# Optimization experiments

Hardware: AMD Instinct MI355X
Metric: run time of the kernel (lower is better)

## Reference

```python
import jax, jax.numpy as jnp
import numpy as np

B, D, L = 32, 64, 8192
K = 512
COMMITMENT_COST = 0.1


def setup_inputs() -> dict:
    key = jax.random.key(0)
    k1, k2 = jax.random.split(key)
    x = jax.random.normal(k1, (B, D, L), dtype=jnp.float32)
    # Embedding initialized uniform(-1/K, 1/K) as in the torch module
    weight = jax.random.uniform(k2, (K, D), dtype=jnp.float32, minval=-1.0 / K, maxval=1.0 / K)
    return {"x": x, "weight": weight}


def reference(x, weight):
    # x: [B, D, L] -> inputs: [B, L, D]
    inputs = jnp.transpose(x, (0, 2, 1))
    flat = inputs.reshape(-1, D)  # [N, D]
    # Squared L2 distances to codebook: [N, K]
    distances = (
        jnp.sum(flat * flat, axis=1, keepdims=True)
        + jnp.sum(weight * weight, axis=1)
        - 2.0 * flat @ weight.T
    )
    encoding_indices = jnp.argmin(distances, axis=1)  # [N]
    # Gather quantized vectors (equivalent to one-hot @ weight)
    quantized = weight[encoding_indices].reshape(inputs.shape)  # [B, L, D]
    e_latent_loss = jnp.mean((jax.lax.stop_gradient(quantized) - inputs) ** 2)
    q_latent_loss = jnp.mean((quantized - jax.lax.stop_gradient(inputs)) ** 2)
    loss = q_latent_loss + COMMITMENT_COST * e_latent_loss
    # Straight-through estimator
    quantized_st = inputs + jax.lax.stop_gradient(quantized - inputs)
    out = jnp.transpose(quantized_st, (0, 2, 1))  # [B, D, L]
    # perplexity = number of unique codes used (jit-friendly via bincount)
    perplexity = jnp.sum(jnp.bincount(encoding_indices, length=K) > 0)
    return (out, loss, perplexity, weight, encoding_indices[:, None])
```

## Files before the change

kernel.cpp:

```cpp
#include <hip/hip_runtime.h>
#include <math.h>

#define BB 32
#define DD 64
#define LL 8192
#define KK 512
#define NN (BB*LL)

#define OUT0_SZ  (BB*DD*LL)
#define LOSS_OFF (OUT0_SZ)
#define PERP_OFF (OUT0_SZ + 1)
#define W_OFF    (OUT0_SZ + 2)
#define IDX_OFF  (W_OFF + KK*DD)

#define WS_TVEC 0
#define WS_HIST 512
#define WS_LACC 1024
#define WS_WPH  1032
#define WS_WPL  (1032 + 16384)

typedef __attribute__((ext_vector_type(4))) float f32x4;
typedef __attribute__((ext_vector_type(8))) short s16x8;
typedef unsigned long long u64;

#define WINDOW 1e-4f

__device__ __forceinline__ unsigned short f2bf(float f) {
  unsigned int u = __float_as_uint(f);
  return (unsigned short)((u + 0x7FFFu + ((u >> 16) & 1u)) >> 16);
}
__device__ __forceinline__ float bf2f(unsigned short s) {
  return __uint_as_float(((unsigned int)s) << 16);
}
__device__ __forceinline__ u64 shflx64(u64 v, int m) {
  unsigned lo = __shfl_xor((unsigned)v, m);
  unsigned hi = __shfl_xor((unsigned)(v >> 32), m);
  return ((u64)hi << 32) | lo;
}
__device__ __forceinline__ unsigned fenc(float f) {
  unsigned u = __float_as_uint(f);
  return (u & 0x80000000u) ? ~u : (u | 0x80000000u);
}
__device__ __forceinline__ float fdec(unsigned e) {
  return __uint_as_float((e & 0x80000000u) ? (e ^ 0x80000000u) : ~e);
}

__global__ void vq_init(const float* __restrict__ w, float* __restrict__ ws,
                        float* __restrict__ dout) {
#pragma clang fp contract(off)
  int t = blockIdx.x * blockDim.x + threadIdx.x;
  if (t < KK) {
    const float* wr = w + t * DD;
    float r[8];
#pragma unroll
    for (int j = 0; j < 8; j++) { float v = wr[j]; r[j] = v * v; }
#pragma unroll
    for (int blk = 8; blk < 64; blk += 8) {
#pragma unroll
      for (int j = 0; j < 8; j++) { float v = wr[blk + j]; float a = v * v; r[j] = r[j] + a; }
    }
    ws[WS_TVEC + t] = ((r[0] + r[1]) + (r[2] + r[3])) + ((r[4] + r[5]) + (r[6] + r[7]));
    ((int*)ws)[WS_HIST + t] = 0;
  }
  if (t == 0) ws[WS_LACC] = 0.0f;

  {
    int j    = t & 7;
    int lane = (t >> 3) & 63;
    int ks   = (t >> 9) & 1;
    int ct   = t >> 10;
    int code = ct * 16 + (lane & 15);
    int d    = ks * 32 + ((lane >> 4) << 3) + j;
    float v  = w[code * DD + d];
    unsigned short h = f2bf(v);
    unsigned short l = f2bf(v - bf2f(h));
    ((unsigned short*)(ws + WS_WPH))[((ct * 2 + ks) * 64 + lane) * 8 + j] = h;
    ((unsigned short*)(ws + WS_WPL))[((ct * 2 + ks) * 64 + lane) * 8 + j] = l;
  }

  if (t < KK * DD / 2) {
    ((float2*)(dout + W_OFF))[t] = ((const float2*)w)[t];
  }
}

__launch_bounds__(256, 2)
__global__ void vq_main(const float* __restrict__ x, const float* __restrict__ w,
                        const float* __restrict__ ws, float* __restrict__ dout) {
#pragma clang fp contract(off)
  __shared__ uint4 xh_lds[4][64][8];
  __shared__ uint4 xl_lds[4][64][8];
  __shared__ float t_lds[KK];
  __shared__ u64   g_lds[256];
  __shared__ unsigned short cand[256][4];
  __shared__ int   ccnt[256];
  __shared__ unsigned char flags[KK];

  const float* tvec = ws + WS_TVEC;
  const s16x8* wph8 = (const s16x8*)(ws + WS_WPH);
  const s16x8* wpl8 = (const s16x8*)(ws + WS_WPL);
  int* hist = (int*)ws + WS_HIST;
  float* lacc = (float*)ws + WS_LACC;

  const int tid  = threadIdx.x;
  const int lane = tid & 63;
  const int wv   = tid >> 6;
  const int res  = lane & 15;

  for (int e = tid; e < KK; e += 256) { t_lds[e] = tvec[e]; flags[e] = 0; }
  ccnt[tid] = 0;

  const int n = blockIdx.x * 256 + wv * 64 + lane;
  const int b = n >> 13, l = n & 8191;
  const float* px = x + (size_t)b * DD * LL + l;

  {
    float xv[64];
#pragma unroll
    for (int i = 0; i < 64; i++) xv[i] = px[(size_t)i * LL];
#pragma unroll
    for (int blk = 0; blk < 8; blk++) {
      unsigned ph[4], pl[4];
#pragma unroll
      for (int q = 0; q < 4; q++) {
        float v0 = xv[blk * 8 + 2 * q],     v1 = xv[blk * 8 + 2 * q + 1];
        unsigned short h0 = f2bf(v0), h1 = f2bf(v1);
        unsigned short l0 = f2bf(v0 - bf2f(h0)), l1 = f2bf(v1 - bf2f(h1));
        ph[q] = (unsigned)h0 | ((unsigned)h1 << 16);
        pl[q] = (unsigned)l0 | ((unsigned)l1 << 16);
      }
      int sw = blk ^ (lane & 7);
      uint4 vh; vh.x = ph[0]; vh.y = ph[1]; vh.z = ph[2]; vh.w = ph[3];
      uint4 vl; vl.x = pl[0]; vl.y = pl[1]; vl.z = pl[2]; vl.w = pl[3];
      xh_lds[wv][lane][sw] = vh;
      xl_lds[wv][lane][sw] = vl;
    }
  }
  __syncthreads();

  s16x8 afh[4][2], afl[4][2];
  {
    const s16x8* xh8 = (const s16x8*)xh_lds;
    const s16x8* xl8 = (const s16x8*)xl_lds;
#pragma unroll
    for (int t2 = 0; t2 < 4; t2++)
#pragma unroll
      for (int ks = 0; ks < 2; ks++) {
        int idx = (wv * 64 + t2 * 16 + (lane & 15)) * 8 + ((ks * 4 + (lane >> 4)) ^ (lane & 7));
        afh[t2][ks] = xh8[idx];
        afl[t2][ks] = xl8[idx];
      }
  }

  float d1[4][4], d2[4][4]; int k1[4][4];
#pragma unroll
  for (int t2 = 0; t2 < 4; t2++)
#pragma unroll
    for (int r = 0; r < 4; r++) { d1[t2][r] = INFINITY; d2[t2][r] = INFINITY; k1[t2][r] = 0; }

  s16x8 bh0 = wph8[lane], bh1 = wph8[64 + lane];
  s16x8 bl0 = wpl8[lane], bl1 = wpl8[64 + lane];
  float tc = t_lds[res];

#pragma clang loop unroll(disable)
  for (int ct = 0; ct < 32; ct++) {
    int cn = (ct + 1) & 31;
    s16x8 nh0 = wph8[cn * 128 + lane],      nh1 = wph8[cn * 128 + 64 + lane];
    s16x8 nl0 = wpl8[cn * 128 + lane],      nl1 = wpl8[cn * 128 + 64 + lane];
    float ntc = t_lds[cn * 16 + res];

#pragma unroll
    for (int t2 = 0; t2 < 4; t2++) {
      f32x4 acc = {0.f, 0.f, 0.f, 0.f};
      acc = __builtin_amdgcn_mfma_f32_16x16x32_bf16(afl[t2][0], bh0, acc, 0, 0, 0);
      acc = __builtin_amdgcn_mfma_f32_16x16x32_bf16(afl[t2][1], bh1, acc, 0, 0, 0);
      acc = __builtin_amdgcn_mfma_f32_16x16x32_bf16(afh[t2][0], bl0, acc, 0, 0, 0);
      acc = __builtin_amdgcn_mfma_f32_16x16x32_bf16(afh[t2][1], bl1, acc, 0, 0, 0);
      acc = __builtin_amdgcn_mfma_f32_16x16x32_bf16(afh[t2][0], bh0, acc, 0, 0, 0);
      acc = __builtin_amdgcn_mfma_f32_16x16x32_bf16(afh[t2][1], bh1, acc, 0, 0, 0);
#pragma unroll
      for (int r = 0; r < 4; r++) {
        float dap = fmaf(-2.0f, acc[r], tc);
        bool c1 = dap < d1[t2][r];
        bool c2 = dap < d2[t2][r];
        d2[t2][r] = c1 ? d1[t2][r] : (c2 ? dap : d2[t2][r]);
        d1[t2][r] = c1 ? dap : d1[t2][r];
        k1[t2][r] = c1 ? ct : k1[t2][r];
      }
    }
    bh0 = nh0; bh1 = nh1; bl0 = nl0; bl1 = nl1; tc = ntc;
  }

  u64 gmin[4][4];
#pragma unroll
  for (int t2 = 0; t2 < 4; t2++)
#pragma unroll
    for (int r = 0; r < 4; r++) {
      u64 pk = (((u64)fenc(d1[t2][r])) << 32) | (u64)(k1[t2][r] * 16 + res);
      u64 q1 = shflx64(pk, 1); pk = pk < q1 ? pk : q1;
      u64 q2 = shflx64(pk, 2); pk = pk < q2 ? pk : q2;
      u64 q4 = shflx64(pk, 4); pk = pk < q4 ? pk : q4;
      u64 q8 = shflx64(pk, 8); pk = pk < q8 ? pk : q8;
      gmin[t2][r] = pk;
    }

#pragma unroll
  for (int t2 = 0; t2 < 4; t2++)
#pragma unroll
    for (int r = 0; r < 4; r++) {
      int row = wv * 64 + t2 * 16 + ((lane >> 4) << 2) + r;
      if (res == 0) g_lds[row] = gmin[t2][r];
      float thr = fdec((unsigned)(gmin[t2][r] >> 32)) + WINDOW;
      bool in1 = d1[t2][r] <= thr;
      bool in2 = d2[t2][r] <= thr;
      if (in1) { int p = atomicAdd(&ccnt[row], 1); if (p < 4) cand[row][p] = (unsigned short)(k1[t2][r] * 16 + res); }
      if (in2) { int p = atomicAdd(&ccnt[row], 1); if (p < 4) cand[row][p] = (unsigned short)(512 + res); }
    }
  __syncthreads();

  float xr[64];
#pragma unroll
  for (int i = 0; i < 64; i++) xr[i] = px[(size_t)i * LL];

  int kwin;
  {
    int row = wv * 64 + lane;
    int cnt = ccnt[row];
    if (cnt <= 1) {
      kwin = (int)(g_lds[row] & 0x1FFu);
    } else {
      float s;
      {
        float r[8];
#pragma unroll
        for (int j = 0; j < 8; j++) r[j] = xr[j] * xr[j];
#pragma unroll
        for (int blk = 8; blk < 64; blk += 8)
#pragma unroll
          for (int j = 0; j < 8; j++) { float a = xr[blk + j] * xr[blk + j]; r[j] = r[j] + a; }
        s = ((r[0] + r[1]) + (r[2] + r[3])) + ((r[4] + r[5]) + (r[6] + r[7]));
      }
      u64 best = ~0ULL;
      auto evalExact = [&](int c) {
        const float4* wr = (const float4*)(w + c * DD);
        float gg = 0.0f;
#pragma unroll
        for (int i = 0; i < 16; i++) {
          float4 wq = wr[i];
          gg = fmaf(xr[4 * i + 0], wq.x, gg); gg = fmaf(xr[4 * i + 1], wq.y, gg);
          gg = fmaf(xr[4 * i + 2], wq.z, gg); gg = fmaf(xr[4 * i + 3], wq.w, gg);
        }
        float de = fmaf(-2.0f, gg, s + t_lds[c]);
        u64 pk = (((u64)__float_as_uint(de)) << 32) | (u64)c;
        if (pk < best) best = pk;
      };
      if (cnt > 4) {
        for (int c = 0; c < KK; c++) evalExact(c);
      } else {
        for (int i = 0; i < cnt; i++) {
          int c = cand[row][i];
          if (c < 512) evalExact(c);
          else { int c0 = c - 512; for (int jj = 0; jj < 32; jj++) evalExact(jj * 16 + c0); }
        }
      }
      kwin = (int)(best & 0x1FFu);
    }
  }

  float ls = 0.0f;
  {
    float* o = dout + (size_t)b * DD * LL + l;
    const float4* wr = (const float4*)(w + kwin * DD);
#pragma unroll
    for (int i = 0; i < 16; i++) {
      float4 v = wr[i];
      o[(size_t)(4 * i + 0) * LL] = v.x; o[(size_t)(4 * i + 1) * LL] = v.y;
      o[(size_t)(4 * i + 2) * LL] = v.z; o[(size_t)(4 * i + 3) * LL] = v.w;
      float df;
      df = v.x - xr[4 * i + 0]; ls = fmaf(df, df, ls);
      df = v.y - xr[4 * i + 1]; ls = fmaf(df, df, ls);
      df = v.z - xr[4 * i + 2]; ls = fmaf(df, df, ls);
      df = v.w - xr[4 * i + 3]; ls = fmaf(df, df, ls);
    }
  }
  dout[IDX_OFF + n] = (float)kwin;
  flags[kwin] = 1;

#pragma unroll
  for (int o = 32; o > 0; o >>= 1) ls += __shfl_down(ls, o);
  if ((tid & 63) == 0) atomicAdd(lacc, ls);

  __syncthreads();
  for (int e = tid; e < KK; e += 256)
    if (flags[e]) atomicOr(&hist[e], 1);
}

__global__ void vq_final(const float* __restrict__ ws, float* __restrict__ dout) {
  __shared__ int red[512];
  const int* hist = (const int*)ws + WS_HIST;
  int tid = threadIdx.x;
  red[tid] = (hist[tid] != 0) ? 1 : 0;
  __syncthreads();
  for (int sx = 256; sx > 0; sx >>= 1) {
    if (tid < sx) red[tid] += red[tid + sx];
    __syncthreads();
  }
  if (tid == 0) {
    dout[PERP_OFF] = (float)red[0];
    float m = ws[WS_LACC] / 16777216.0f;
    dout[LOSS_OFF] = m + 0.1f * m;
  }
}

extern "C" void kernel_launch(void* const* d_in, const int* in_sizes, int n_in,
                              void* d_out, int out_size, void* d_ws, size_t ws_size,
                              hipStream_t stream) {
  const float* x = (const float*)d_in[0];
  const float* w = (const float*)d_in[1];
  float* dout = (float*)d_out;
  float* ws = (float*)d_ws;

  vq_init<<<128, 256, 0, stream>>>(w, ws, dout);
  vq_main<<<NN / 256, 256, 0, stream>>>(x, w, ws, dout);
  vq_final<<<1, 512, 0, stream>>>(ws, dout);
}
```

Before: 246.9 us.

## Share one LDS staging buffer for hi/lo bf16 splits and hoist x reload

Replaces the separate hi and lo LDS staging buffers with a single buffer reused in two passes: the hi halves are written, read into registers, then the lo halves are written and read. This halves that LDS footprint, which may let more blocks fit per CU, at the cost of two extra block barriers. The x reload for the refinement phase is moved ahead of the candidate-reduction code behind a sched_barrier so its global latency overlaps the shuffle and atomic work, which raises register pressure during that phase.

```diff
diff --git a/kernel.cpp b/kernel.cpp
--- a/kernel.cpp
+++ b/kernel.cpp
@@ -87,8 +87,7 @@
 __global__ void vq_main(const float* __restrict__ x, const float* __restrict__ w,
                         const float* __restrict__ ws, float* __restrict__ dout) {
 #pragma clang fp contract(off)
-  __shared__ uint4 xh_lds[4][64][8];
-  __shared__ uint4 xl_lds[4][64][8];
+  __shared__ uint4 xs_lds[4][64][8];
   __shared__ float t_lds[KK];
   __shared__ u64   g_lds[256];
   __shared__ unsigned short cand[256][4];
@@ -113,42 +112,61 @@
   const int b = n >> 13, l = n & 8191;
   const float* px = x + (size_t)b * DD * LL + l;
 
+  s16x8 afh[4][2], afl[4][2];
   {
     float xv[64];
 #pragma unroll
     for (int i = 0; i < 64; i++) xv[i] = px[(size_t)i * LL];
+
 #pragma unroll
     for (int blk = 0; blk < 8; blk++) {
-      unsigned ph[4], pl[4];
+      unsigned ph[4];
 #pragma unroll
       for (int q = 0; q < 4; q++) {
-        float v0 = xv[blk * 8 + 2 * q],     v1 = xv[blk * 8 + 2 * q + 1];
-        unsigned short h0 = f2bf(v0), h1 = f2bf(v1);
-        unsigned short l0 = f2bf(v0 - bf2f(h0)), l1 = f2bf(v1 - bf2f(h1));
-        ph[q] = (unsigned)h0 | ((unsigned)h1 << 16);
-        pl[q] = (unsigned)l0 | ((unsigned)l1 << 16);
+        float v0 = xv[blk * 8 + 2 * q], v1 = xv[blk * 8 + 2 * q + 1];
+        ph[q] = (unsigned)f2bf(v0) | ((unsigned)f2bf(v1) << 16);
       }
       int sw = blk ^ (lane & 7);
       uint4 vh; vh.x = ph[0]; vh.y = ph[1]; vh.z = ph[2]; vh.w = ph[3];
+      xs_lds[wv][lane][sw] = vh;
+    }
+    __syncthreads();
+    {
+      const s16x8* xs8 = (const s16x8*)xs_lds;
+#pragma unroll
+      for (int t2 = 0; t2 < 4; t2++)
+#pragma unroll
+        for (int ks = 0; ks < 2; ks++) {
+          int idx = (wv * 64 + t2 * 16 + (lane & 15)) * 8 + ((ks * 4 + (lane >> 4)) ^ (lane & 7));
+          afh[t2][ks] = xs8[idx];
+        }
+    }
+    __syncthreads();
+
+#pragma unroll
+    for (int blk = 0; blk < 8; blk++) {
+      unsigned pl[4];
+#pragma unroll
+      for (int q = 0; q < 4; q++) {
+        float v0 = xv[blk * 8 + 2 * q],     h0f = bf2f(f2bf(v0));
+        float v1 = xv[blk * 8 + 2 * q + 1], h1f = bf2f(f2bf(v1));
+        pl[q] = (unsigned)f2bf(v0 - h0f) | ((unsigned)f2bf(v1 - h1f) << 16);
+      }
+      int sw = blk ^ (lane & 7);
       uint4 vl; vl.x = pl[0]; vl.y = pl[1]; vl.z = pl[2]; vl.w = pl[3];
-      xh_lds[wv][lane][sw] = vh;
-      xl_lds[wv][lane][sw] = vl;
-    }
-  }
-  __syncthreads();
-
-  s16x8 afh[4][2], afl[4][2];
-  {
-    const s16x8* xh8 = (const s16x8*)xh_lds;
-    const s16x8* xl8 = (const s16x8*)xl_lds;
-#pragma unroll
-    for (int t2 = 0; t2 < 4; t2++)
-#pragma unroll
-      for (int ks = 0; ks < 2; ks++) {
-        int idx = (wv * 64 + t2 * 16 + (lane & 15)) * 8 + ((ks * 4 + (lane >> 4)) ^ (lane & 7));
-        afh[t2][ks] = xh8[idx];
-        afl[t2][ks] = xl8[idx];
-      }
+      xs_lds[wv][lane][sw] = vl;
+    }
+    __syncthreads();
+    {
+      const s16x8* xs8 = (const s16x8*)xs_lds;
+#pragma unroll
+      for (int t2 = 0; t2 < 4; t2++)
+#pragma unroll
+        for (int ks = 0; ks < 2; ks++) {
+          int idx = (wv * 64 + t2 * 16 + (lane & 15)) * 8 + ((ks * 4 + (lane >> 4)) ^ (lane & 7));
+          afl[t2][ks] = xs8[idx];
+        }
+    }
   }
 
   float d1[4][4], d2[4][4]; int k1[4][4];
@@ -190,6 +208,11 @@
     bh0 = nh0; bh1 = nh1; bl0 = nl0; bl1 = nl1; tc = ntc;
   }
 
+  __builtin_amdgcn_sched_barrier(0);
+  float xr[64];
+#pragma unroll
+  for (int i = 0; i < 64; i++) xr[i] = px[(size_t)i * LL];
+
   u64 gmin[4][4];
 #pragma unroll
   for (int t2 = 0; t2 < 4; t2++)
@@ -216,10 +239,6 @@
       if (in2) { int p = atomicAdd(&ccnt[row], 1); if (p < 4) cand[row][p] = (unsigned short)(512 + res); }
     }
   __syncthreads();
-
-  float xr[64];
-#pragma unroll
-  for (int i = 0; i < 64; i++) xr[i] = px[(size_t)i * LL];
 
   int kwin;
   {
```

After: 236.8 us. 4.1% less time.

## Drop x low-part MFMAs, widen rescore window, raise occupancy target

Applied to the files above, without the earlier changes.

Removes the bf16 low-part split of x, so each distance tile uses four MFMAs instead of six and x staging in LDS halves. The candidate window is widened to absorb the larger approximation error, and exact fp32 rescoring still picks the winner. The top-2 tracking becomes branchless min/max, x is reloaded only when rescoring or when computing the loss, and launch bounds target three blocks per CU to cut register pressure. The risks are more rows falling into the slow exact-rescore path and possible spills under the tighter register budget.

```diff
diff --git a/kernel.cpp b/kernel.cpp
--- a/kernel.cpp
+++ b/kernel.cpp
@@ -23,7 +23,7 @@
 typedef __attribute__((ext_vector_type(8))) short s16x8;
 typedef unsigned long long u64;
 
-#define WINDOW 1e-4f
+#define WINDOW 5e-4f
 
 __device__ __forceinline__ unsigned short f2bf(float f) {
   unsigned int u = __float_as_uint(f);
@@ -83,12 +83,11 @@
   }
 }
 
-__launch_bounds__(256, 2)
+__launch_bounds__(256, 3)
 __global__ void vq_main(const float* __restrict__ x, const float* __restrict__ w,
                         const float* __restrict__ ws, float* __restrict__ dout) {
 #pragma clang fp contract(off)
-  __shared__ uint4 xh_lds[4][64][8];
-  __shared__ uint4 xl_lds[4][64][8];
+  __shared__ uint4 xs_lds[4][64][8];
   __shared__ float t_lds[KK];
   __shared__ u64   g_lds[256];
   __shared__ unsigned short cand[256][4];
@@ -119,35 +118,28 @@
     for (int i = 0; i < 64; i++) xv[i] = px[(size_t)i * LL];
 #pragma unroll
     for (int blk = 0; blk < 8; blk++) {
-      unsigned ph[4], pl[4];
+      unsigned ph[4];
 #pragma unroll
       for (int q = 0; q < 4; q++) {
-        float v0 = xv[blk * 8 + 2 * q],     v1 = xv[blk * 8 + 2 * q + 1];
-        unsigned short h0 = f2bf(v0), h1 = f2bf(v1);
-        unsigned short l0 = f2bf(v0 - bf2f(h0)), l1 = f2bf(v1 - bf2f(h1));
-        ph[q] = (unsigned)h0 | ((unsigned)h1 << 16);
-        pl[q] = (unsigned)l0 | ((unsigned)l1 << 16);
+        float v0 = xv[blk * 8 + 2 * q], v1 = xv[blk * 8 + 2 * q + 1];
+        ph[q] = (unsigned)f2bf(v0) | ((unsigned)f2bf(v1) << 16);
       }
       int sw = blk ^ (lane & 7);
       uint4 vh; vh.x = ph[0]; vh.y = ph[1]; vh.z = ph[2]; vh.w = ph[3];
-      uint4 vl; vl.x = pl[0]; vl.y = pl[1]; vl.z = pl[2]; vl.w = pl[3];
-      xh_lds[wv][lane][sw] = vh;
-      xl_lds[wv][lane][sw] = vl;
+      xs_lds[wv][lane][sw] = vh;
     }
   }
   __syncthreads();
 
-  s16x8 afh[4][2], afl[4][2];
-  {
-    const s16x8* xh8 = (const s16x8*)xh_lds;
-    const s16x8* xl8 = (const s16x8*)xl_lds;
+  s16x8 afh[4][2];
+  {
+    const s16x8* xs8 = (const s16x8*)xs_lds;
 #pragma unroll
     for (int t2 = 0; t2 < 4; t2++)
 #pragma unroll
       for (int ks = 0; ks < 2; ks++) {
         int idx = (wv * 64 + t2 * 16 + (lane & 15)) * 8 + ((ks * 4 + (lane >> 4)) ^ (lane & 7));
-        afh[t2][ks] = xh8[idx];
-        afl[t2][ks] = xl8[idx];
+        afh[t2][ks] = xs8[idx];
       }
   }
 
@@ -171,8 +163,6 @@
 #pragma unroll
     for (int t2 = 0; t2 < 4; t2++) {
       f32x4 acc = {0.f, 0.f, 0.f, 0.f};
-      acc = __builtin_amdgcn_mfma_f32_16x16x32_bf16(afl[t2][0], bh0, acc, 0, 0, 0);
-      acc = __builtin_amdgcn_mfma_f32_16x16x32_bf16(afl[t2][1], bh1, acc, 0, 0, 0);
       acc = __builtin_amdgcn_mfma_f32_16x16x32_bf16(afh[t2][0], bl0, acc, 0, 0, 0);
       acc = __builtin_amdgcn_mfma_f32_16x16x32_bf16(afh[t2][1], bl1, acc, 0, 0, 0);
       acc = __builtin_amdgcn_mfma_f32_16x16x32_bf16(afh[t2][0], bh0, acc, 0, 0, 0);
@@ -180,11 +170,11 @@
 #pragma unroll
       for (int r = 0; r < 4; r++) {
         float dap = fmaf(-2.0f, acc[r], tc);
+        float m  = fmaxf(d1[t2][r], dap);
+        d2[t2][r] = fminf(d2[t2][r], m);
         bool c1 = dap < d1[t2][r];
-        bool c2 = dap < d2[t2][r];
-        d2[t2][r] = c1 ? d1[t2][r] : (c2 ? dap : d2[t2][r]);
-        d1[t2][r] = c1 ? dap : d1[t2][r];
         k1[t2][r] = c1 ? ct : k1[t2][r];
+        d1[t2][r] = fminf(d1[t2][r], dap);
       }
     }
     bh0 = nh0; bh1 = nh1; bl0 = nl0; bl1 = nl1; tc = ntc;
@@ -217,10 +207,6 @@
     }
   __syncthreads();
 
-  float xr[64];
-#pragma unroll
-  for (int i = 0; i < 64; i++) xr[i] = px[(size_t)i * LL];
-
   int kwin;
   {
     int row = wv * 64 + lane;
@@ -228,6 +214,9 @@
     if (cnt <= 1) {
       kwin = (int)(g_lds[row] & 0x1FFu);
     } else {
+      float xr[64];
+#pragma unroll
+      for (int i = 0; i < 64; i++) xr[i] = px[(size_t)i * LL];
       float s;
       {
         float r[8];
@@ -273,13 +262,17 @@
 #pragma unroll
     for (int i = 0; i < 16; i++) {
       float4 v = wr[i];
+      float xa = px[(size_t)(4 * i + 0) * LL];
+      float xb = px[(size_t)(4 * i + 1) * LL];
+      float xc = px[(size_t)(4 * i + 2) * LL];
+      float xd = px[(size_t)(4 * i + 3) * LL];
       o[(size_t)(4 * i + 0) * LL] = v.x; o[(size_t)(4 * i + 1) * LL] = v.y;
       o[(size_t)(4 * i + 2) * LL] = v.z; o[(size_t)(4 * i + 3) * LL] = v.w;
       float df;
-      df = v.x - xr[4 * i + 0]; ls = fmaf(df, df, ls);
-      df = v.y - xr[4 * i + 1]; ls = fmaf(df, df, ls);
-      df = v.z - xr[4 * i + 2]; ls = fmaf(df, df, ls);
-      df = v.w - xr[4 * i + 3]; ls = fmaf(df, df, ls);
+      df = v.x - xa; ls = fmaf(df, df, ls);
+      df = v.y - xb; ls = fmaf(df, df, ls);
+      df = v.z - xc; ls = fmaf(df, df, ls);
+      df = v.w - xd; ls = fmaf(df, df, ls);
     }
   }
   dout[IDX_OFF + n] = (float)kwin;
```

Result: slower. 528.0 us (+113.9%).
